# Optimization experiments

Hardware: AMD Instinct MI355X
Metric: run time of the kernel (lower is better)

Reference implementation:

```python
import jax, jax.numpy as jnp
import numpy as np

BETA = 0.9      # snntorch Leaky decay
THRESH = 1.0    # default threshold
SLOPE = 25.0    # fast_sigmoid surrogate slope

# Heaviside spike with fast_sigmoid surrogate gradient: d/dx = 1/(slope*|x|+1)^2
@jax.custom_vjp
def spike_fn(x):
    return (x > 0).astype(x.dtype)

def _spike_fwd(x):
    return (x > 0).astype(x.dtype), x

def _spike_bwd(x, g):
    return (g / (SLOPE * jnp.abs(x) + 1.0) ** 2,)

spike_fn.defvjp(_spike_fwd, _spike_bwd)

def setup_inputs() -> dict:
    key = jax.random.key(0)
    k0, k1, k2 = jax.random.split(key, 3)
    B, T, F, H, C = 8192, 200, 40, 128, 5
    x = jax.random.normal(k0, (B, T, F), dtype=jnp.float32)
    w1 = jax.random.normal(k1, (H, F), dtype=jnp.float32) / np.sqrt(F).astype(np.float32)
    b1 = jnp.zeros((H,), jnp.float32)
    w2 = jax.random.normal(k2, (C, H), dtype=jnp.float32) / np.sqrt(H).astype(np.float32)
    b2 = jnp.zeros((C,), jnp.float32)
    return {"x": x, "w1": w1, "b1": b1, "w2": w2, "b2": b2}

def reference(x, w1, b1, w2, b2):
    # x: [B, T, F] -> time-major [T, B, F] (matches x.permute(1,0,2))
    xt = jnp.transpose(x, (1, 0, 2))
    B = x.shape[0]
    mem1 = jnp.zeros((B, w1.shape[0]), x.dtype)
    mem2 = jnp.zeros((B, w2.shape[0]), x.dtype)

    def step(carry, x_t):
        m1, m2 = carry
        cur1 = x_t @ w1.T + b1                       # [B, 128]
        # snntorch Leaky, reset_mechanism='subtract'; reset is detached
        reset1 = jax.lax.stop_gradient((m1 > THRESH).astype(x_t.dtype))
        m1 = BETA * m1 + cur1 - reset1 * THRESH
        spk1 = spike_fn(m1 - THRESH)
        cur2 = spk1 @ w2.T + b2                      # [B, 5]
        reset2 = jax.lax.stop_gradient((m2 > THRESH).astype(x_t.dtype))
        m2 = BETA * m2 + cur2 - reset2 * THRESH
        spk2 = spike_fn(m2 - THRESH)
        return (m1, m2), spk2

    _, spk2_rec = jax.lax.scan(step, (mem1, mem2), xt)
    return spk2_rec  # [T, B, 5], like torch.stack(spk2_rec, dim=0)
```

## Files before the change

kernel.cpp:

```cpp
#include <hip/hip_runtime.h>
#include <cstdint>

#define T_STEPS 200
#define B_TOTAL 8192
#define F_IN    40
#define H_DIM   128
#define C_OUT   5

#define CH      8
#define NCHUNK  (T_STEPS / CH)
#define CHB     (CH * F_IN * 4)
#define WIN     2048
#define ROWB    (T_STEPS * F_IN * 4)

typedef float v2f __attribute__((ext_vector_type(2)));
typedef float v4f __attribute__((ext_vector_type(4)));

#define PKFMA_LO(acc, xp, wp)                                                  \
    asm("v_pk_fma_f32 %0, %1, %2, %0 op_sel:[0,0,0] op_sel_hi:[0,1,1]"        \
        : "+v"(acc) : "v"(xp), "v"(wp))
#define PKFMA_HI(acc, xp, wp)                                                  \
    asm("v_pk_fma_f32 %0, %1, %2, %0 op_sel:[1,0,0] op_sel_hi:[1,1,1]"        \
        : "+v"(acc) : "v"(xp), "v"(wp))

__device__ __forceinline__ void gload_lds16(const void* g, void* l) {
    __builtin_amdgcn_global_load_lds(
        (const __attribute__((address_space(1))) void*)g,
        (__attribute__((address_space(3))) void*)l, 16, 0, 0);
}

__global__ __launch_bounds__(256, 4)
void snn_l1(const float* __restrict__ x,
            const float* __restrict__ w1,
            const float* __restrict__ b1,
            ulonglong2* __restrict__ masks)
{
    __shared__ __align__(16) char xs[2][4][WIN];

    const int li = threadIdx.x & 63;
    const int wv = threadIdx.x >> 6;
    const int b  = blockIdx.x * 4 + wv;
    const int hA = li, hB = li + 64;

    v2f wab[F_IN];
    {
        const float* wArow = w1 + hA * F_IN;
        const float* wBrow = w1 + hB * F_IN;
#pragma unroll
        for (int f = 0; f < F_IN; ++f) {
            v2f p; p.x = wArow[f]; p.y = wBrow[f];
            wab[f] = p;
        }
    }
#pragma unroll
    for (int f = 0; f < F_IN; ++f) asm("" : "+v"(wab[f]));

    const float b1A = b1[hA], b1B = b1[hB];
    float mA = 0.0f, mB = 0.0f, rA = 0.0f, rB = 0.0f;

    const char* xb = (const char*)x + (size_t)b * ROWB + (size_t)li * 16;

    auto winstart = [](int c) { return (c == NCHUNK - 1) ? (ROWB - WIN) : c * CHB; };

    gload_lds16(xb + winstart(0),        &xs[0][wv][0]);
    gload_lds16(xb + winstart(0) + 1024, &xs[0][wv][1024]);
    asm volatile("s_waitcnt vmcnt(0)" ::: "memory");

    ulonglong2* mp = masks + b;

    for (int c = 0; c < NCHUNK; ++c) {
        if (c + 1 < NCHUNK) {
            const int ws = winstart(c + 1);
            gload_lds16(xb + ws,        &xs[(c + 1) & 1][wv][0]);
            gload_lds16(xb + ws + 1024, &xs[(c + 1) & 1][wv][1024]);
        }
        const int delta = c * CHB - winstart(c);
        const char* xsw = &xs[c & 1][wv][0];

#pragma unroll
        for (int sp = 0; sp < CH; sp += 2) {
            const v4f* xr0 = (const v4f*)(xsw + delta + (sp + 0) * (F_IN * 4));
            const v4f* xr1 = (const v4f*)(xsw + delta + (sp + 1) * (F_IN * 4));
            v2f acc0 = {0.0f, 0.0f};
            v2f acc1 = {0.0f, 0.0f};
#pragma unroll
            for (int q = 0; q < 10; ++q) {
                const v4f x0 = xr0[q];
                const v4f x1 = xr1[q];
                const v2f x0lo = x0.lo, x0hi = x0.hi;
                const v2f x1lo = x1.lo, x1hi = x1.hi;
                PKFMA_LO(acc0, x0lo, wab[4*q+0]);
                PKFMA_LO(acc1, x1lo, wab[4*q+0]);
                PKFMA_HI(acc0, x0lo, wab[4*q+1]);
                PKFMA_HI(acc1, x1lo, wab[4*q+1]);
                PKFMA_LO(acc0, x0hi, wab[4*q+2]);
                PKFMA_LO(acc1, x1hi, wab[4*q+2]);
                PKFMA_HI(acc0, x0hi, wab[4*q+3]);
                PKFMA_HI(acc1, x1hi, wab[4*q+3]);
            }
            mA = __fsub_rn(__fadd_rn(__fmul_rn(0.9f, mA), __fadd_rn(acc0.x, b1A)), rA);
            mB = __fsub_rn(__fadd_rn(__fmul_rn(0.9f, mB), __fadd_rn(acc0.y, b1B)), rB);
            bool sA = mA > 1.0f, sB = mB > 1.0f;
            rA = sA ? 1.0f : 0.0f;
            rB = sB ? 1.0f : 0.0f;
            unsigned long long lo = __ballot(sA);
            unsigned long long hi = __ballot(sB);
            if (li == 0) *mp = make_ulonglong2(lo, hi);
            mp += B_TOTAL;
            mA = __fsub_rn(__fadd_rn(__fmul_rn(0.9f, mA), __fadd_rn(acc1.x, b1A)), rA);
            mB = __fsub_rn(__fadd_rn(__fmul_rn(0.9f, mB), __fadd_rn(acc1.y, b1B)), rB);
            sA = mA > 1.0f; sB = mB > 1.0f;
            rA = sA ? 1.0f : 0.0f;
            rB = sB ? 1.0f : 0.0f;
            lo = __ballot(sA);
            hi = __ballot(sB);
            if (li == 0) *mp = make_ulonglong2(lo, hi);
            mp += B_TOTAL;
        }
        asm volatile("s_waitcnt vmcnt(0)" ::: "memory");
    }
}

__global__ __launch_bounds__(256)
void snn_l2a(const ulonglong2* __restrict__ masks,
             const float* __restrict__ w2,
             float* __restrict__ cur2)
{
    __shared__ float w2s[H_DIM * C_OUT];
    const int tid = threadIdx.x;
    for (int i = tid; i < H_DIM * C_OUT; i += 256) {
        const int c = i / H_DIM, h = i % H_DIM;
        w2s[h * C_OUT + c] = w2[i];
    }
    __syncthreads();

    const size_t gid = (size_t)blockIdx.x * 256 + tid;
    const ulonglong2 mk = masks[gid];
    float s0 = 0.f, s1 = 0.f, s2 = 0.f, s3 = 0.f, s4 = 0.f;

    auto acc32 = [&](uint32_t w, int base) {
        while (w) {
            const int h = base + __builtin_ctz(w);
            w &= w - 1;
            const float* wp = &w2s[h * C_OUT];
            s0 = __fadd_rn(s0, wp[0]);
            s1 = __fadd_rn(s1, wp[1]);
            s2 = __fadd_rn(s2, wp[2]);
            s3 = __fadd_rn(s3, wp[3]);
            s4 = __fadd_rn(s4, wp[4]);
        }
    };
    acc32((uint32_t)(mk.x & 0xffffffffull), 0);
    acc32((uint32_t)(mk.x >> 32), 32);
    acc32((uint32_t)(mk.y & 0xffffffffull), 64);
    acc32((uint32_t)(mk.y >> 32), 96);

    float* o = cur2 + gid * C_OUT;
    o[0] = s0; o[1] = s1; o[2] = s2; o[3] = s3; o[4] = s4;
}

__global__ __launch_bounds__(256)
void snn_l2b(const float* __restrict__ cur2,
             const float* __restrict__ b2,
             float* __restrict__ out)
{
    const int gid = blockIdx.x * 256 + threadIdx.x;
    const float b2c = b2[gid % 5];
    const int STRIDE = B_TOTAL * C_OUT;
    float m2 = 0.0f, r2 = 0.0f;

    float f0 = cur2[0 * (size_t)STRIDE + gid];
    float f1 = cur2[1 * (size_t)STRIDE + gid];
    float f2 = cur2[2 * (size_t)STRIDE + gid];
    float f3 = cur2[3 * (size_t)STRIDE + gid];

#define L2B_STEP(F, TT)                                                        \
    {                                                                          \
        const float cur = __fadd_rn(F, b2c);                                   \
        m2 = __fsub_rn(__fadd_rn(__fmul_rn(0.9f, m2), cur), r2);               \
        const float s = (m2 > 1.0f) ? 1.0f : 0.0f;                             \
        r2 = s;                                                                \
        out[(size_t)(TT) * STRIDE + gid] = s;                                  \
        F = ((TT) + 4 < T_STEPS) ? cur2[(size_t)((TT) + 4) * STRIDE + gid]     \
                                 : 0.0f;                                       \
    }

    for (int t = 0; t < T_STEPS; t += 4) {
        L2B_STEP(f0, t + 0)
        L2B_STEP(f1, t + 1)
        L2B_STEP(f2, t + 2)
        L2B_STEP(f3, t + 3)
    }
#undef L2B_STEP
}

extern "C" void kernel_launch(void* const* d_in, const int* in_sizes, int n_in,
                              void* d_out, int out_size, void* d_ws, size_t ws_size,
                              hipStream_t stream) {
    const float* x  = (const float*)d_in[0];
    const float* w1 = (const float*)d_in[1];
    const float* b1 = (const float*)d_in[2];
    const float* w2 = (const float*)d_in[3];
    const float* b2 = (const float*)d_in[4];
    float* out = (float*)d_out;

    ulonglong2* masks = (ulonglong2*)d_ws;
    float* cur2 = (float*)((char*)d_ws + (size_t)T_STEPS * B_TOTAL * 16);

    snn_l1 <<<dim3(B_TOTAL / 4),             dim3(256), 0, stream>>>(x, w1, b1, masks);
    snn_l2a<<<dim3(T_STEPS * B_TOTAL / 256), dim3(256), 0, stream>>>(masks, w2, cur2);
    snn_l2b<<<dim3(B_TOTAL * C_OUT / 256),   dim3(256), 0, stream>>>(cur2, b2, out);
}
```

Baseline: 292.2 us.

## Process two batch rows per wave in layer-1 kernel for independent recurrences

Each wave now handles two batch rows instead of one, loading both rows' input windows into doubled LDS buffers. The two membrane recurrences are independent, so their FMA chains and ballots can interleave, and both masks are written together, with half as many blocks launched. The aim is to hide the serial dependence of the time recurrence and reuse the register-resident weights across two rows. In exchange, LDS use per block doubles (which may lower occupancy), more state is kept in registers, and the register-pinning asm for the weights is dropped.

Measured after the change: 294.2 us. No clear change (+0.7%).

```diff
diff --git a/kernel.cpp b/kernel.cpp
--- a/kernel.cpp
+++ b/kernel.cpp
@@ -35,11 +35,11 @@
             const float* __restrict__ b1,
             ulonglong2* __restrict__ masks)
 {
-    __shared__ __align__(16) char xs[2][4][WIN];
+    __shared__ __align__(16) char xs[2][4][2][WIN];
 
     const int li = threadIdx.x & 63;
     const int wv = threadIdx.x >> 6;
-    const int b  = blockIdx.x * 4 + wv;
+    const int b0 = blockIdx.x * 8 + wv * 2;
     const int hA = li, hB = li + 64;
 
     v2f wab[F_IN];
@@ -52,35 +52,38 @@
             wab[f] = p;
         }
     }
-#pragma unroll
-    for (int f = 0; f < F_IN; ++f) asm("" : "+v"(wab[f]));
-
     const float b1A = b1[hA], b1B = b1[hB];
-    float mA = 0.0f, mB = 0.0f, rA = 0.0f, rB = 0.0f;
-
-    const char* xb = (const char*)x + (size_t)b * ROWB + (size_t)li * 16;
+    float mA0 = 0.f, mB0 = 0.f, rA0 = 0.f, rB0 = 0.f;
+    float mA1 = 0.f, mB1 = 0.f, rA1 = 0.f, rB1 = 0.f;
+
+    const char* xb0 = (const char*)x + (size_t)b0 * ROWB + (size_t)li * 16;
+    const char* xb1 = xb0 + ROWB;
 
     auto winstart = [](int c) { return (c == NCHUNK - 1) ? (ROWB - WIN) : c * CHB; };
 
-    gload_lds16(xb + winstart(0),        &xs[0][wv][0]);
-    gload_lds16(xb + winstart(0) + 1024, &xs[0][wv][1024]);
+    gload_lds16(xb0 + winstart(0),        &xs[0][wv][0][0]);
+    gload_lds16(xb0 + winstart(0) + 1024, &xs[0][wv][0][1024]);
+    gload_lds16(xb1 + winstart(0),        &xs[0][wv][1][0]);
+    gload_lds16(xb1 + winstart(0) + 1024, &xs[0][wv][1][1024]);
     asm volatile("s_waitcnt vmcnt(0)" ::: "memory");
 
-    ulonglong2* mp = masks + b;
+    ulonglong2* mp = masks + b0;
 
     for (int c = 0; c < NCHUNK; ++c) {
         if (c + 1 < NCHUNK) {
             const int ws = winstart(c + 1);
-            gload_lds16(xb + ws,        &xs[(c + 1) & 1][wv][0]);
-            gload_lds16(xb + ws + 1024, &xs[(c + 1) & 1][wv][1024]);
+            gload_lds16(xb0 + ws,        &xs[(c + 1) & 1][wv][0][0]);
+            gload_lds16(xb0 + ws + 1024, &xs[(c + 1) & 1][wv][0][1024]);
+            gload_lds16(xb1 + ws,        &xs[(c + 1) & 1][wv][1][0]);
+            gload_lds16(xb1 + ws + 1024, &xs[(c + 1) & 1][wv][1][1024]);
         }
         const int delta = c * CHB - winstart(c);
-        const char* xsw = &xs[c & 1][wv][0];
+        const char* xsw = &xs[c & 1][wv][0][0];
 
 #pragma unroll
-        for (int sp = 0; sp < CH; sp += 2) {
-            const v4f* xr0 = (const v4f*)(xsw + delta + (sp + 0) * (F_IN * 4));
-            const v4f* xr1 = (const v4f*)(xsw + delta + (sp + 1) * (F_IN * 4));
+        for (int s = 0; s < CH; ++s) {
+            const v4f* xr0 = (const v4f*)(xsw + delta + s * (F_IN * 4));
+            const v4f* xr1 = (const v4f*)(xsw + WIN + delta + s * (F_IN * 4));
             v2f acc0 = {0.0f, 0.0f};
             v2f acc1 = {0.0f, 0.0f};
 #pragma unroll
@@ -98,23 +101,24 @@
                 PKFMA_HI(acc0, x0hi, wab[4*q+3]);
                 PKFMA_HI(acc1, x1hi, wab[4*q+3]);
             }
-            mA = __fsub_rn(__fadd_rn(__fmul_rn(0.9f, mA), __fadd_rn(acc0.x, b1A)), rA);
-            mB = __fsub_rn(__fadd_rn(__fmul_rn(0.9f, mB), __fadd_rn(acc0.y, b1B)), rB);
-            bool sA = mA > 1.0f, sB = mB > 1.0f;
-            rA = sA ? 1.0f : 0.0f;
-            rB = sB ? 1.0f : 0.0f;
-            unsigned long long lo = __ballot(sA);
-            unsigned long long hi = __ballot(sB);
-            if (li == 0) *mp = make_ulonglong2(lo, hi);
-            mp += B_TOTAL;
-            mA = __fsub_rn(__fadd_rn(__fmul_rn(0.9f, mA), __fadd_rn(acc1.x, b1A)), rA);
-            mB = __fsub_rn(__fadd_rn(__fmul_rn(0.9f, mB), __fadd_rn(acc1.y, b1B)), rB);
-            sA = mA > 1.0f; sB = mB > 1.0f;
-            rA = sA ? 1.0f : 0.0f;
-            rB = sB ? 1.0f : 0.0f;
-            lo = __ballot(sA);
-            hi = __ballot(sB);
-            if (li == 0) *mp = make_ulonglong2(lo, hi);
+            mA0 = __fsub_rn(__fadd_rn(__fmul_rn(0.9f, mA0), __fadd_rn(acc0.x, b1A)), rA0);
+            mB0 = __fsub_rn(__fadd_rn(__fmul_rn(0.9f, mB0), __fadd_rn(acc0.y, b1B)), rB0);
+            bool sA0 = mA0 > 1.0f, sB0 = mB0 > 1.0f;
+            rA0 = sA0 ? 1.0f : 0.0f;
+            rB0 = sB0 ? 1.0f : 0.0f;
+            const unsigned long long lo0 = __ballot(sA0);
+            const unsigned long long hi0 = __ballot(sB0);
+            mA1 = __fsub_rn(__fadd_rn(__fmul_rn(0.9f, mA1), __fadd_rn(acc1.x, b1A)), rA1);
+            mB1 = __fsub_rn(__fadd_rn(__fmul_rn(0.9f, mB1), __fadd_rn(acc1.y, b1B)), rB1);
+            bool sA1 = mA1 > 1.0f, sB1 = mB1 > 1.0f;
+            rA1 = sA1 ? 1.0f : 0.0f;
+            rB1 = sB1 ? 1.0f : 0.0f;
+            const unsigned long long lo1 = __ballot(sA1);
+            const unsigned long long hi1 = __ballot(sB1);
+            if (li == 0) {
+                mp[0] = make_ulonglong2(lo0, hi0);
+                mp[1] = make_ulonglong2(lo1, hi1);
+            }
             mp += B_TOTAL;
         }
         asm volatile("s_waitcnt vmcnt(0)" ::: "memory");
@@ -207,7 +211,7 @@
     ulonglong2* masks = (ulonglong2*)d_ws;
     float* cur2 = (float*)((char*)d_ws + (size_t)T_STEPS * B_TOTAL * 16);
 
-    snn_l1 <<<dim3(B_TOTAL / 4),             dim3(256), 0, stream>>>(x, w1, b1, masks);
+    snn_l1 <<<dim3(B_TOTAL / 8),             dim3(256), 0, stream>>>(x, w1, b1, masks);
     snn_l2a<<<dim3(T_STEPS * B_TOTAL / 256), dim3(256), 0, stream>>>(masks, w2, cur2);
     snn_l2b<<<dim3(B_TOTAL * C_OUT / 256),   dim3(256), 0, stream>>>(cur2, b2, out);
 }
```
